# Kernel tuning notes

Hardware: AMD Instinct MI355X
Metric: run time of the kernel (lower is better)

## Reference

```python
import jax, jax.numpy as jnp
import numpy as np

INPUT_LEN = 24
HIDDEN = 64
BATCH = 8192


def _lstm_layer(seq, Wih, Whh, bih, bhh):
    """Single torch-style LSTM layer. seq: [T, B, in] -> hs: [T, B, H].
    Gate order matches torch: i, f, g, o."""
    B = seq.shape[1]
    H = Whh.shape[1]
    b = bih + bhh
    h0 = jnp.zeros((B, H), seq.dtype)
    c0 = jnp.zeros((B, H), seq.dtype)

    def step(carry, x_t):
        h, c = carry
        gates = x_t @ Wih.T + h @ Whh.T + b  # [B, 4H]
        i, f, g, o = jnp.split(gates, 4, axis=-1)
        c = jax.nn.sigmoid(f) * c + jax.nn.sigmoid(i) * jnp.tanh(g)
        h = jax.nn.sigmoid(o) * jnp.tanh(c)
        return (h, c), h

    _, hs = jax.lax.scan(step, (h0, c0), seq)
    return hs


def setup_inputs() -> dict:
    key = jax.random.key(0)
    ks = jax.random.split(key, 16)
    H = HIDDEN
    s = 1.0 / np.sqrt(H)  # torch LSTM/Linear init scale
    u = lambda k, shape, sc: jax.random.uniform(k, shape, jnp.float32, -sc, sc)
    return {
        "x": jax.random.normal(ks[0], (BATCH, INPUT_LEN), jnp.float32),
        # LSTM layer 0 (input size 1)
        "Wih0": u(ks[1], (4 * H, 1), s),
        "Whh0": u(ks[2], (4 * H, H), s),
        "bih0": u(ks[3], (4 * H,), s),
        "bhh0": u(ks[4], (4 * H,), s),
        # LSTM layer 1 (input size H)
        "Wih1": u(ks[5], (4 * H, H), s),
        "Whh1": u(ks[6], (4 * H, H), s),
        "bih1": u(ks[7], (4 * H,), s),
        "bhh1": u(ks[8], (4 * H,), s),
        # predictor MLP: Linear(H,32) -> ReLU -> Linear(32,1)
        "W1": u(ks[9], (32, H), s),
        "b1": u(ks[10], (32,), s),
        "W2": u(ks[11], (1, 32), 1.0 / np.sqrt(32)),
        "b2": u(ks[12], (1,), 1.0 / np.sqrt(32)),
        "damping": jnp.asarray(0.1, jnp.float32),
        "steps": 20,
    }


def reference(x, Wih0, Whh0, bih0, bhh0, Wih1, Whh1, bih1, bhh1,
              W1, b1, W2, b2, damping, steps):
    cur = x[..., None]  # [B, T, 1]
    alpha = jax.nn.sigmoid(damping)
    preds = []
    prev = None
    for _ in range(steps):
        seq = jnp.transpose(cur, (1, 0, 2))  # [T, B, 1]
        h1 = _lstm_layer(seq, Wih0, Whh0, bih0, bhh0)   # [T, B, H]
        h2 = _lstm_layer(h1, Wih1, Whh1, bih1, bhh1)     # [T, B, H]
        last = h2[-1]                                     # [B, H]
        pred = jax.nn.relu(last @ W1.T + b1) @ W2.T + b2  # [B, 1]
        if prev is not None:
            # torch: pred*(1-alpha) + predictions[-1].detach()*alpha*0.5
            pred = pred * (1.0 - alpha) + jax.lax.stop_gradient(prev) * alpha * 0.5
        preds.append(pred)
        prev = pred
        cur = jnp.concatenate([cur[:, 1:, :], pred[:, None, :]], axis=1)
    return jnp.concatenate(preds, axis=1)  # [B, steps]
```

## Files before the change

kernel.cpp:

```cpp
#include <hip/hip_runtime.h>


typedef _Float16 f16x8 __attribute__((ext_vector_type(8)));
typedef float f32x4 __attribute__((ext_vector_type(4)));

#define NBLK 256
#define NTHR 512
#define SRB  160

__device__ __forceinline__ float rcp_(float x) { return __builtin_amdgcn_rcpf(x); }
__device__ __forceinline__ float exp2_(float x) { return __builtin_amdgcn_exp2f(x); }
__device__ __forceinline__ f32x4 mfma16(uint4 a, uint4 b, f32x4 c) {
  return __builtin_amdgcn_mfma_f32_16x16x32_f16(
      __builtin_bit_cast(f16x8, a), __builtin_bit_cast(f16x8, b), c, 0, 0, 0);
}
__device__ __forceinline__ uint4 pack8s(const float* p, float s) {
  union { uint4 u; _Float16 h[8]; } r;
  #pragma unroll
  for (int i = 0; i < 8; ++i) r.h[i] = (_Float16)(p[i] * s);
  return r.u;
}
__device__ __forceinline__ float gatestep(float aI, float aF, float aG, float aO,
                                          float& cst) {
  float xx = exp2_(-aI), xf = exp2_(-aF), yy = exp2_(-aG), xo = exp2_(-aO);
  float P = (1.0f + xx) * (1.0f + yy);
  float Q = 1.0f + xf;
  float N = fmaf(cst, P * Q - P * xf, (1.0f - yy) * Q);
  float cv = N * rcp_(P * Q);
  cst = cv;
  float z = exp2_(-2.88539008178f * cv);
  return (1.0f - z) * rcp_((1.0f + xo) * (1.0f + z));
}

__global__ __launch_bounds__(NTHR, 2) void lstm_forecast(
    const float* __restrict__ x,
    const float* __restrict__ Wih0, const float* __restrict__ Whh0,
    const float* __restrict__ bih0, const float* __restrict__ bhh0,
    const float* __restrict__ Wih1, const float* __restrict__ Whh1,
    const float* __restrict__ bih1, const float* __restrict__ bhh1,
    const float* __restrict__ W1,   const float* __restrict__ b1,
    const float* __restrict__ W2,   const float* __restrict__ b2,
    const float* __restrict__ damping, const int* __restrict__ stepsPtr,
    float* __restrict__ out)
{
  __shared__ __align__(16) _Float16 h1s[2][2][1280];
  __shared__ __align__(16) _Float16 h2s[2][2][1280];
  __shared__ __align__(16) float    win[2][24 * 16];
  __shared__ float pm[2][2][16];
  __shared__ int   cnt[2];

  const int tid  = threadIdx.x;
  const int wave = tid >> 6;
  const int lane = tid & 63;
  const int cc   = lane & 15;
  const int hi   = lane >> 4;
  const int g    = wave >> 2;
  const int wg   = wave & 3;
  const int b0g  = blockIdx.x * 32 + g * 16;
  const float L2E = 1.44269504089f;

  uint4 wB0[4][2], wB1[4][2], wB2[4][2];
  float bias0v[4], wih0v[4];
  f32x4 bi1[4];
  #pragma unroll
  for (int gt = 0; gt < 4; ++gt) {
    float sc = (gt == 2) ? 2.0f * L2E : L2E;
    int row = (wg + 4 * gt) * 16 + cc;
    #pragma unroll
    for (int f = 0; f < 2; ++f) {
      int col = f * 32 + hi * 8;
      wB0[gt][f] = pack8s(Whh0 + row * 64 + col, sc);
      wB1[gt][f] = pack8s(Wih1 + row * 64 + col, sc);
      wB2[gt][f] = pack8s(Whh1 + row * 64 + col, sc);
    }
    bias0v[gt] = (bih0[row] + bhh0[row]) * sc;
    wih0v[gt]  = Wih0[row] * sc;
    float b1c  = (bih1[row] + bhh1[row]) * sc;
    #pragma unroll
    for (int r = 0; r < 4; ++r) bi1[gt][r] = b1c;
  }
  uint4 wM[2];
  {
    int row = (wg & 1) * 16 + cc;
    wM[0] = pack8s(W1 + row * 64 + hi * 8, 1.0f);
    wM[1] = pack8s(W1 + row * 64 + 32 + hi * 8, 1.0f);
  }
  const float w2v  = W2[(wg & 1) * 16 + cc];
  const float b1vv = b1[(wg & 1) * 16 + cc];
  const float alpha  = rcp_(1.0f + exp2_(-L2E * damping[0]));
  const int   nsteps = stepsPtr[0];
  const float b2v    = b2[0];

  for (int e = (tid & 255); e < 384; e += 256) {
    int b = e & 15, t = e >> 4;
    win[g][t * 16 + b] = x[(b0g + b) * 24 + t];
  }
  if (tid < 2) cnt[tid] = 0;
  __syncthreads();

  int syncTgt = 0;
  auto gsync = [&]() {
    syncTgt += 4;
    if (lane == 0)
      __hip_atomic_fetch_add(&cnt[g], 1, __ATOMIC_RELEASE,
                             __HIP_MEMORY_SCOPE_WORKGROUP);
    while (__hip_atomic_load(&cnt[g], __ATOMIC_ACQUIRE,
                             __HIP_MEMORY_SCOPE_WORKGROUP) < syncTgt) { }
  };

  char* h1b[2] = { (char*)h1s[g][0], (char*)h1s[g][1] };
  char* h2b[2] = { (char*)h2s[g][0], (char*)h2s[g][1] };
  float* winw = win[g];
  const int offA = cc * SRB + hi * 16;
  const int offS = (wg * 16 + cc) * 2;
  float prevp = 0.0f;

  for (int s = 0; s < nsteps; ++s) {
    float c1[4] = {0, 0, 0, 0}, c2s[4] = {0, 0, 0, 0};

    {
      float4 xw = *(const float4*)&winw[(s % 24) * 16 + hi * 4];
      float xa[4] = {xw.x, xw.y, xw.z, xw.w};
      #pragma unroll
      for (int r = 0; r < 4; ++r) {
        float hv = gatestep(fmaf(xa[r], wih0v[0], bias0v[0]),
                            fmaf(xa[r], wih0v[1], bias0v[1]),
                            fmaf(xa[r], wih0v[2], bias0v[2]),
                            fmaf(xa[r], wih0v[3], bias0v[3]), c1[r]);
        *(_Float16*)(h1b[0] + (hi * 4 + r) * SRB + offS) = (_Float16)hv;
      }
    }
    gsync();
    uint4 a1lo = *(const uint4*)(h1b[0] + offA);
    uint4 a1hi = *(const uint4*)(h1b[0] + offA + 64);
    uint4 a2lo = make_uint4(0, 0, 0, 0), a2hi = make_uint4(0, 0, 0, 0);

    for (int t = 0; t < 23; ++t) {
      int pb = (t + 1) & 1;
      int ph = s + t + 1; if (ph >= 24) ph -= 24;
      float4 xw = *(const float4*)&winw[ph * 16 + hi * 4];
      float xa[4] = {xw.x, xw.y, xw.z, xw.w};

      f32x4 acc1[4], acc0[4];
      #pragma unroll
      for (int gt = 0; gt < 4; ++gt) {
        f32x4 tv = mfma16(a1lo, wB1[gt][0], bi1[gt]);
        tv = mfma16(a1hi, wB1[gt][1], tv);
        tv = mfma16(a2lo, wB2[gt][0], tv);
        acc1[gt] = mfma16(a2hi, wB2[gt][1], tv);
      }
      #pragma unroll
      for (int gt = 0; gt < 4; ++gt) {
        f32x4 ai;
        #pragma unroll
        for (int r = 0; r < 4; ++r) ai[r] = fmaf(xa[r], wih0v[gt], bias0v[gt]);
        f32x4 tv = mfma16(a1lo, wB0[gt][0], ai);
        acc0[gt] = mfma16(a1hi, wB0[gt][1], tv);
      }

      char* h2d = h2b[pb];
      char* h1d = h1b[pb];
      #pragma unroll
      for (int r = 0; r < 4; ++r) {
        float hv = gatestep(acc1[0][r], acc1[1][r], acc1[2][r], acc1[3][r], c2s[r]);
        *(_Float16*)(h2d + (hi * 4 + r) * SRB + offS) = (_Float16)hv;
      }
      #pragma unroll
      for (int r = 0; r < 4; ++r) {
        float hv = gatestep(acc0[0][r], acc0[1][r], acc0[2][r], acc0[3][r], c1[r]);
        *(_Float16*)(h1d + (hi * 4 + r) * SRB + offS) = (_Float16)hv;
      }
      gsync();
      a1lo = *(const uint4*)(h1b[pb] + offA);
      a1hi = *(const uint4*)(h1b[pb] + offA + 64);
      a2lo = *(const uint4*)(h2b[pb] + offA);
      a2hi = *(const uint4*)(h2b[pb] + offA + 64);
    }

    {
      f32x4 acc1[4];
      #pragma unroll
      for (int gt = 0; gt < 4; ++gt) {
        f32x4 tv = mfma16(a1lo, wB1[gt][0], bi1[gt]);
        tv = mfma16(a1hi, wB1[gt][1], tv);
        tv = mfma16(a2lo, wB2[gt][0], tv);
        acc1[gt] = mfma16(a2hi, wB2[gt][1], tv);
      }
      #pragma unroll
      for (int r = 0; r < 4; ++r) {
        float cv = c2s[r];
        float hv = gatestep(acc1[0][r], acc1[1][r], acc1[2][r], acc1[3][r], cv);
        *(_Float16*)(h2b[0] + (hi * 4 + r) * SRB + offS) = (_Float16)hv;
      }
    }
    gsync();

    if (wg < 2) {
      uint4 hflo = *(const uint4*)(h2b[0] + offA);
      uint4 hfhi = *(const uint4*)(h2b[0] + offA + 64);
      f32x4 am;
      #pragma unroll
      for (int r = 0; r < 4; ++r) am[r] = b1vv;
      am = mfma16(hflo, wM[0], am);
      am = mfma16(hfhi, wM[1], am);
      float yp[4];
      #pragma unroll
      for (int r = 0; r < 4; ++r) yp[r] = fmaxf(am[r], 0.0f) * w2v;
      #pragma unroll
      for (int mask = 1; mask <= 8; mask <<= 1) {
        #pragma unroll
        for (int r = 0; r < 4; ++r) yp[r] += __shfl_xor(yp[r], mask);
      }
      if (cc == 0) {
        #pragma unroll
        for (int r = 0; r < 4; ++r) pm[g][wg][hi * 4 + r] = yp[r];
      }
    }
    gsync();

    if (wg == 0 && lane < 16) {
      float y = pm[g][0][lane] + pm[g][1][lane] + b2v;
      float pd = (s == 0) ? y : fmaf(y, 1.0f - alpha, prevp * (alpha * 0.5f));
      prevp = pd;
      winw[(s % 24) * 16 + lane] = pd;
      out[(long)(b0g + lane) * nsteps + s] = pd;
    }
    gsync();
  }
}

extern "C" void kernel_launch(void* const* d_in, const int* in_sizes, int n_in,
                              void* d_out, int out_size, void* d_ws, size_t ws_size,
                              hipStream_t stream) {
  (void)in_sizes; (void)n_in; (void)out_size; (void)d_ws; (void)ws_size;
  lstm_forecast<<<NBLK, NTHR, 0, stream>>>(
      (const float*)d_in[0],
      (const float*)d_in[1],  (const float*)d_in[2],
      (const float*)d_in[3],  (const float*)d_in[4],
      (const float*)d_in[5],  (const float*)d_in[6],
      (const float*)d_in[7],  (const float*)d_in[8],
      (const float*)d_in[9],  (const float*)d_in[10],
      (const float*)d_in[11], (const float*)d_in[12],
      (const float*)d_in[13], (const int*)d_in[14],
      (float*)d_out);
}
```

Before: 661.6 us.

## Use one batch group per block with hardware barriers instead of atomic spin sync

Each 512-thread block held two independent 16-row batch groups that synchronised with LDS atomic counters and spin loops. Now each 256-thread block holds a single group and uses __syncthreads, with twice as many blocks launched. The LDS row stride for the h buffers shrinks from 160 to 144 bytes, which changes the bank-conflict pattern. In gatestep, P*Q - P*xf is replaced by the algebraically equal P, which saves arithmetic on the recurrent critical path. The trade-off is losing the ability of the two groups in a block to drift independently of each other's barriers.

```diff
diff --git a/kernel.cpp b/kernel.cpp
--- a/kernel.cpp
+++ b/kernel.cpp
@@ -4,9 +4,9 @@
 typedef _Float16 f16x8 __attribute__((ext_vector_type(8)));
 typedef float f32x4 __attribute__((ext_vector_type(4)));
 
-#define NBLK 256
-#define NTHR 512
-#define SRB  160
+#define NBLK 512
+#define NTHR 256
+#define SRB  144
 
 __device__ __forceinline__ float rcp_(float x) { return __builtin_amdgcn_rcpf(x); }
 __device__ __forceinline__ float exp2_(float x) { return __builtin_amdgcn_exp2f(x); }
@@ -25,7 +25,7 @@
   float xx = exp2_(-aI), xf = exp2_(-aF), yy = exp2_(-aG), xo = exp2_(-aO);
   float P = (1.0f + xx) * (1.0f + yy);
   float Q = 1.0f + xf;
-  float N = fmaf(cst, P * Q - P * xf, (1.0f - yy) * Q);
+  float N = fmaf(cst, P, (1.0f - yy) * Q);
   float cv = N * rcp_(P * Q);
   cst = cv;
   float z = exp2_(-2.88539008178f * cv);
@@ -43,20 +43,17 @@
     const float* __restrict__ damping, const int* __restrict__ stepsPtr,
     float* __restrict__ out)
 {
-  __shared__ __align__(16) _Float16 h1s[2][2][1280];
-  __shared__ __align__(16) _Float16 h2s[2][2][1280];
-  __shared__ __align__(16) float    win[2][24 * 16];
-  __shared__ float pm[2][2][16];
-  __shared__ int   cnt[2];
+  __shared__ __align__(16) char h1s[2][16 * SRB];
+  __shared__ __align__(16) char h2s[2][16 * SRB];
+  __shared__ __align__(16) float win[24 * 16];
+  __shared__ __align__(16) float pm[2][16];
 
   const int tid  = threadIdx.x;
   const int wave = tid >> 6;
   const int lane = tid & 63;
   const int cc   = lane & 15;
   const int hi   = lane >> 4;
-  const int g    = wave >> 2;
-  const int wg   = wave & 3;
-  const int b0g  = blockIdx.x * 32 + g * 16;
+  const int b0g  = blockIdx.x * 16;
   const float L2E = 1.44269504089f;
 
   uint4 wB0[4][2], wB1[4][2], wB2[4][2];
@@ -65,7 +62,7 @@
   #pragma unroll
   for (int gt = 0; gt < 4; ++gt) {
     float sc = (gt == 2) ? 2.0f * L2E : L2E;
-    int row = (wg + 4 * gt) * 16 + cc;
+    int row = (wave + 4 * gt) * 16 + cc;
     #pragma unroll
     for (int f = 0; f < 2; ++f) {
       int col = f * 32 + hi * 8;
@@ -81,45 +78,31 @@
   }
   uint4 wM[2];
   {
-    int row = (wg & 1) * 16 + cc;
+    int row = (wave & 1) * 16 + cc;
     wM[0] = pack8s(W1 + row * 64 + hi * 8, 1.0f);
     wM[1] = pack8s(W1 + row * 64 + 32 + hi * 8, 1.0f);
   }
-  const float w2v  = W2[(wg & 1) * 16 + cc];
-  const float b1vv = b1[(wg & 1) * 16 + cc];
+  const float w2v  = W2[(wave & 1) * 16 + cc];
+  const float b1vv = b1[(wave & 1) * 16 + cc];
   const float alpha  = rcp_(1.0f + exp2_(-L2E * damping[0]));
   const int   nsteps = stepsPtr[0];
   const float b2v    = b2[0];
 
-  for (int e = (tid & 255); e < 384; e += 256) {
+  for (int e = tid; e < 384; e += NTHR) {
     int b = e & 15, t = e >> 4;
-    win[g][t * 16 + b] = x[(b0g + b) * 24 + t];
-  }
-  if (tid < 2) cnt[tid] = 0;
+    win[t * 16 + b] = x[(b0g + b) * 24 + t];
+  }
   __syncthreads();
 
-  int syncTgt = 0;
-  auto gsync = [&]() {
-    syncTgt += 4;
-    if (lane == 0)
-      __hip_atomic_fetch_add(&cnt[g], 1, __ATOMIC_RELEASE,
-                             __HIP_MEMORY_SCOPE_WORKGROUP);
-    while (__hip_atomic_load(&cnt[g], __ATOMIC_ACQUIRE,
-                             __HIP_MEMORY_SCOPE_WORKGROUP) < syncTgt) { }
-  };
-
-  char* h1b[2] = { (char*)h1s[g][0], (char*)h1s[g][1] };
-  char* h2b[2] = { (char*)h2s[g][0], (char*)h2s[g][1] };
-  float* winw = win[g];
   const int offA = cc * SRB + hi * 16;
-  const int offS = (wg * 16 + cc) * 2;
+  const int offS = (wave * 16 + cc) * 2;
   float prevp = 0.0f;
 
   for (int s = 0; s < nsteps; ++s) {
     float c1[4] = {0, 0, 0, 0}, c2s[4] = {0, 0, 0, 0};
 
     {
-      float4 xw = *(const float4*)&winw[(s % 24) * 16 + hi * 4];
+      float4 xw = *(const float4*)&win[(s % 24) * 16 + hi * 4];
       float xa[4] = {xw.x, xw.y, xw.z, xw.w};
       #pragma unroll
       for (int r = 0; r < 4; ++r) {
@@ -127,18 +110,18 @@
                             fmaf(xa[r], wih0v[1], bias0v[1]),
                             fmaf(xa[r], wih0v[2], bias0v[2]),
                             fmaf(xa[r], wih0v[3], bias0v[3]), c1[r]);
-        *(_Float16*)(h1b[0] + (hi * 4 + r) * SRB + offS) = (_Float16)hv;
-      }
-    }
-    gsync();
-    uint4 a1lo = *(const uint4*)(h1b[0] + offA);
-    uint4 a1hi = *(const uint4*)(h1b[0] + offA + 64);
+        *(_Float16*)(h1s[0] + (hi * 4 + r) * SRB + offS) = (_Float16)hv;
+      }
+    }
+    __syncthreads();
+    uint4 a1lo = *(const uint4*)(h1s[0] + offA);
+    uint4 a1hi = *(const uint4*)(h1s[0] + offA + 64);
     uint4 a2lo = make_uint4(0, 0, 0, 0), a2hi = make_uint4(0, 0, 0, 0);
 
     for (int t = 0; t < 23; ++t) {
       int pb = (t + 1) & 1;
       int ph = s + t + 1; if (ph >= 24) ph -= 24;
-      float4 xw = *(const float4*)&winw[ph * 16 + hi * 4];
+      float4 xw = *(const float4*)&win[ph * 16 + hi * 4];
       float xa[4] = {xw.x, xw.y, xw.z, xw.w};
 
       f32x4 acc1[4], acc0[4];
@@ -158,8 +141,8 @@
         acc0[gt] = mfma16(a1hi, wB0[gt][1], tv);
       }
 
-      char* h2d = h2b[pb];
-      char* h1d = h1b[pb];
+      char* h2d = h2s[pb];
+      char* h1d = h1s[pb];
       #pragma unroll
       for (int r = 0; r < 4; ++r) {
         float hv = gatestep(acc1[0][r], acc1[1][r], acc1[2][r], acc1[3][r], c2s[r]);
@@ -170,11 +153,11 @@
         float hv = gatestep(acc0[0][r], acc0[1][r], acc0[2][r], acc0[3][r], c1[r]);
         *(_Float16*)(h1d + (hi * 4 + r) * SRB + offS) = (_Float16)hv;
       }
-      gsync();
-      a1lo = *(const uint4*)(h1b[pb] + offA);
-      a1hi = *(const uint4*)(h1b[pb] + offA + 64);
-      a2lo = *(const uint4*)(h2b[pb] + offA);
-      a2hi = *(const uint4*)(h2b[pb] + offA + 64);
+      __syncthreads();
+      a1lo = *(const uint4*)(h1s[pb] + offA);
+      a1hi = *(const uint4*)(h1s[pb] + offA + 64);
+      a2lo = *(const uint4*)(h2s[pb] + offA);
+      a2hi = *(const uint4*)(h2s[pb] + offA + 64);
     }
 
     {
@@ -190,14 +173,14 @@
       for (int r = 0; r < 4; ++r) {
         float cv = c2s[r];
         float hv = gatestep(acc1[0][r], acc1[1][r], acc1[2][r], acc1[3][r], cv);
-        *(_Float16*)(h2b[0] + (hi * 4 + r) * SRB + offS) = (_Float16)hv;
-      }
-    }
-    gsync();
-
-    if (wg < 2) {
-      uint4 hflo = *(const uint4*)(h2b[0] + offA);
-      uint4 hfhi = *(const uint4*)(h2b[0] + offA + 64);
+        *(_Float16*)(h2s[0] + (hi * 4 + r) * SRB + offS) = (_Float16)hv;
+      }
+    }
+    __syncthreads();
+
+    if (wave < 2) {
+      uint4 hflo = *(const uint4*)(h2s[0] + offA);
+      uint4 hfhi = *(const uint4*)(h2s[0] + offA + 64);
       f32x4 am;
       #pragma unroll
       for (int r = 0; r < 4; ++r) am[r] = b1vv;
@@ -213,19 +196,19 @@
       }
       if (cc == 0) {
         #pragma unroll
-        for (int r = 0; r < 4; ++r) pm[g][wg][hi * 4 + r] = yp[r];
-      }
-    }
-    gsync();
-
-    if (wg == 0 && lane < 16) {
-      float y = pm[g][0][lane] + pm[g][1][lane] + b2v;
+        for (int r = 0; r < 4; ++r) pm[wave][hi * 4 + r] = yp[r];
+      }
+    }
+    __syncthreads();
+
+    if (wave == 0 && lane < 16) {
+      float y = pm[0][lane] + pm[1][lane] + b2v;
       float pd = (s == 0) ? y : fmaf(y, 1.0f - alpha, prevp * (alpha * 0.5f));
       prevp = pd;
-      winw[(s % 24) * 16 + lane] = pd;
+      win[(s % 24) * 16 + lane] = pd;
       out[(long)(b0g + lane) * nsteps + s] = pd;
     }
-    gsync();
+    __syncthreads();
   }
 }
 
```

After: 597.0 us. 9.8% less time.

## Replace per-group LDS atomic spin barriers with block barriers and retune LDS padding

Applied to the files above, without the earlier changes.

Swaps the per-half-block spin barrier (an LDS atomic increment plus a polling loop) for hardware __syncthreads across the whole 512-thread block. The aim is to remove the polling and atomic traffic, at the cost of tying the two independent 16-row batch groups to a single barrier. It also changes the LDS row stride for the h1/h2 tiles from 160 to 144 bytes to alter the bank-conflict pattern. Finally, it simplifies the cell-state coefficient in gatestep, since P*Q - P*xf equals P, which saves a few flops per gate step.

```diff
diff --git a/kernel.cpp b/kernel.cpp
--- a/kernel.cpp
+++ b/kernel.cpp
@@ -6,7 +6,7 @@
 
 #define NBLK 256
 #define NTHR 512
-#define SRB  160
+#define SRB  144
 
 __device__ __forceinline__ float rcp_(float x) { return __builtin_amdgcn_rcpf(x); }
 __device__ __forceinline__ float exp2_(float x) { return __builtin_amdgcn_exp2f(x); }
@@ -25,7 +25,7 @@
   float xx = exp2_(-aI), xf = exp2_(-aF), yy = exp2_(-aG), xo = exp2_(-aO);
   float P = (1.0f + xx) * (1.0f + yy);
   float Q = 1.0f + xf;
-  float N = fmaf(cst, P * Q - P * xf, (1.0f - yy) * Q);
+  float N = fmaf(cst, P, (1.0f - yy) * Q);
   float cv = N * rcp_(P * Q);
   cst = cv;
   float z = exp2_(-2.88539008178f * cv);
@@ -43,20 +43,19 @@
     const float* __restrict__ damping, const int* __restrict__ stepsPtr,
     float* __restrict__ out)
 {
-  __shared__ __align__(16) _Float16 h1s[2][2][1280];
-  __shared__ __align__(16) _Float16 h2s[2][2][1280];
-  __shared__ __align__(16) float    win[2][24 * 16];
-  __shared__ float pm[2][2][16];
-  __shared__ int   cnt[2];
+  __shared__ __align__(16) char h1s[2][2][16 * SRB];
+  __shared__ __align__(16) char h2s[2][2][16 * SRB];
+  __shared__ __align__(16) float win[2][24 * 16];
+  __shared__ __align__(16) float pm[2][2][16];
 
   const int tid  = threadIdx.x;
   const int wave = tid >> 6;
   const int lane = tid & 63;
   const int cc   = lane & 15;
   const int hi   = lane >> 4;
-  const int g    = wave >> 2;
+  const int q    = wave >> 2;
   const int wg   = wave & 3;
-  const int b0g  = blockIdx.x * 32 + g * 16;
+  const int b0g  = blockIdx.x * 32 + q * 16;
   const float L2E = 1.44269504089f;
 
   uint4 wB0[4][2], wB1[4][2], wB2[4][2];
@@ -91,26 +90,17 @@
   const int   nsteps = stepsPtr[0];
   const float b2v    = b2[0];
 
-  for (int e = (tid & 255); e < 384; e += 256) {
-    int b = e & 15, t = e >> 4;
-    win[g][t * 16 + b] = x[(b0g + b) * 24 + t];
-  }
-  if (tid < 2) cnt[tid] = 0;
+  for (int e = tid; e < 768; e += NTHR) {
+    int qq  = (e >= 384) ? 1 : 0;
+    int rem = e - qq * 384;
+    int b = rem & 15, t = rem >> 4;
+    win[qq][t * 16 + b] = x[(blockIdx.x * 32 + qq * 16 + b) * 24 + t];
+  }
   __syncthreads();
 
-  int syncTgt = 0;
-  auto gsync = [&]() {
-    syncTgt += 4;
-    if (lane == 0)
-      __hip_atomic_fetch_add(&cnt[g], 1, __ATOMIC_RELEASE,
-                             __HIP_MEMORY_SCOPE_WORKGROUP);
-    while (__hip_atomic_load(&cnt[g], __ATOMIC_ACQUIRE,
-                             __HIP_MEMORY_SCOPE_WORKGROUP) < syncTgt) { }
-  };
-
-  char* h1b[2] = { (char*)h1s[g][0], (char*)h1s[g][1] };
-  char* h2b[2] = { (char*)h2s[g][0], (char*)h2s[g][1] };
-  float* winw = win[g];
+  char* h1b[2] = { h1s[q][0], h1s[q][1] };
+  char* h2b[2] = { h2s[q][0], h2s[q][1] };
+  float* winw  = win[q];
   const int offA = cc * SRB + hi * 16;
   const int offS = (wg * 16 + cc) * 2;
   float prevp = 0.0f;
@@ -130,7 +120,7 @@
         *(_Float16*)(h1b[0] + (hi * 4 + r) * SRB + offS) = (_Float16)hv;
       }
     }
-    gsync();
+    __syncthreads();
     uint4 a1lo = *(const uint4*)(h1b[0] + offA);
     uint4 a1hi = *(const uint4*)(h1b[0] + offA + 64);
     uint4 a2lo = make_uint4(0, 0, 0, 0), a2hi = make_uint4(0, 0, 0, 0);
@@ -170,7 +160,7 @@
         float hv = gatestep(acc0[0][r], acc0[1][r], acc0[2][r], acc0[3][r], c1[r]);
         *(_Float16*)(h1d + (hi * 4 + r) * SRB + offS) = (_Float16)hv;
       }
-      gsync();
+      __syncthreads();
       a1lo = *(const uint4*)(h1b[pb] + offA);
       a1hi = *(const uint4*)(h1b[pb] + offA + 64);
       a2lo = *(const uint4*)(h2b[pb] + offA);
@@ -193,7 +183,7 @@
         *(_Float16*)(h2b[0] + (hi * 4 + r) * SRB + offS) = (_Float16)hv;
       }
     }
-    gsync();
+    __syncthreads();
 
     if (wg < 2) {
       uint4 hflo = *(const uint4*)(h2b[0] + offA);
@@ -213,19 +203,19 @@
       }
       if (cc == 0) {
         #pragma unroll
-        for (int r = 0; r < 4; ++r) pm[g][wg][hi * 4 + r] = yp[r];
-      }
-    }
-    gsync();
+        for (int r = 0; r < 4; ++r) pm[q][wg][hi * 4 + r] = yp[r];
+      }
+    }
+    __syncthreads();
 
     if (wg == 0 && lane < 16) {
-      float y = pm[g][0][lane] + pm[g][1][lane] + b2v;
+      float y = pm[q][0][lane] + pm[q][1][lane] + b2v;
       float pd = (s == 0) ? y : fmaf(y, 1.0f - alpha, prevp * (alpha * 0.5f));
       prevp = pd;
       winw[(s % 24) * 16 + lane] = pd;
       out[(long)(b0g + lane) * nsteps + s] = pd;
     }
-    gsync();
+    __syncthreads();
   }
 }
 
```

After: 642.1 us. 2.9% less time.
